# Performance work log

Measured on AMD Instinct MI355X. Metric: run time of the kernel, lower is better.

## Reference

```python
import jax, jax.numpy as jnp
import numpy as np
import math


def setup_inputs() -> dict:
    key = jax.random.key(0)
    k0, k1, k2, k3, k4 = jax.random.split(key, 5)
    in_f, out_f, nb = 512, 512, 8
    B, S = 4, 2048
    x = jax.random.normal(k0, (B, S, in_f), dtype=jnp.float32)
    # RBF params (frozen in original: basis_trainable=False)
    fan_in = in_f  # fan_in of rbf.weight.T which is (num_basis, in_features)
    bound = 1.0 / math.sqrt(fan_in)
    rbf_weight = jax.random.uniform(k1, (in_f, nb), dtype=jnp.float32,
                                    minval=-math.sqrt(3.0) * 0.33 / math.sqrt(fan_in),
                                    maxval=math.sqrt(3.0) * 0.33 / math.sqrt(fan_in))
    rbf_centers = jnp.tile(jnp.linspace(-bound, bound, nb, dtype=jnp.float32)[None, :], (in_f, 1))
    # KAN spline weight (in, nb, out); fan_in for init is in_f*nb
    fan2 = in_f * nb
    wb = math.sqrt(3.0) * 0.33 / math.sqrt(fan2)
    weight = jax.random.uniform(k2, (in_f, nb, out_f), dtype=jnp.float32, minval=-wb, maxval=wb)
    bias = jax.random.uniform(k3, (out_f,), dtype=jnp.float32,
                              minval=-1.0 / math.sqrt(fan2), maxval=1.0 / math.sqrt(fan2))
    scale_base = jax.random.uniform(k4, (in_f, out_f), dtype=jnp.float32, minval=-0.1, maxval=0.1)
    return {"x": x, "rbf_weight": rbf_weight, "rbf_centers": rbf_centers,
            "weight": weight, "bias": bias, "scale_base": scale_base}


def reference(x, rbf_weight, rbf_centers, weight, bias, scale_base):
    in_f = x.shape[-1]
    nb = rbf_weight.shape[1]
    beta = (nb / math.log2(nb)) ** 2  # get_rbf_width(2/nb, log2(nb))
    batch_shape = x.shape[:-1]
    xf = x.reshape(-1, in_f)  # (N, in)
    # RBF basis expansion: (N, in, nb)
    z = xf[:, :, None] * rbf_weight[None, :, :] - rbf_centers[None, :, :]
    phi = jnp.exp(-beta * (z * z))
    # spline contraction + base path, expressed as efficient contractions
    y = jnp.einsum('nib,ibo->no', phi, weight)
    y = y + bias + jnp.cos(xf) @ scale_base
    return y.reshape(*batch_shape, weight.shape[-1])
```

## Files before the change

kernel.cpp:

```cpp
#include <hip/hip_runtime.h>
#include <hip/hip_bf16.h>

typedef __attribute__((ext_vector_type(8))) short short8;
typedef __attribute__((ext_vector_type(4))) float f32x4;

#define IN_F 512
#define OUT_F 512
#define BM 64
#define BN 256
#define BK 64
#define PHI_STEPS 64
#define NSTEPS 72
#define NT 2
#define IMG_CHUNKS 2048
#define ACH 512
#define A_SH (BM * BK)
#define B_SH (BN * BK)
#define PART_ELEMS (8192 * OUT_F)
#define C2 (-10.2591705f)

__device__ __forceinline__ short f2bf(float f) {
  unsigned u = __builtin_bit_cast(unsigned, f);
  u += 0x7fffu + ((u >> 16) & 1u);
  return (short)(u >> 16);
}

__device__ __forceinline__ void glds16(const void* g, void* l) {
  __builtin_amdgcn_global_load_lds(
      (const __attribute__((address_space(1))) unsigned int*)g,
      (__attribute__((address_space(3))) unsigned int*)l, 16, 0, 0);
}

__device__ __forceinline__ float bsrc(const float* __restrict__ w,
                                      const float* __restrict__ sb,
                                      int k, int col) {
  return (k < IN_F * 8) ? w[(size_t)k * OUT_F + col]
                        : sb[(size_t)(k - IN_F * 8) * OUT_F + col];
}

__global__ void __launch_bounds__(256) prep_b(const float* __restrict__ w,
                                              const float* __restrict__ sb,
                                              short* __restrict__ img) {
  const int D = blockIdx.x * 256 + threadIdx.x;
  const int ci = D & (IMG_CHUNKS - 1);
  const int im = D >> 11;
  const int s = im % NSTEPS;
  const int nt = im / NSTEPS;
  const int n = ci >> 3, slot = ci & 7;
  const int oct = slot ^ (n & 7);
  const int col = nt * BN + n;
  short8 v;
#pragma unroll
  for (int j = 0; j < 8; ++j) v[j] = f2bf(bsrc(w, sb, s * 64 + oct * 8 + j, col));
  *(short8*)&img[(size_t)D * 8] = v;
}

__global__ void __launch_bounds__(256) prep_a(const float* __restrict__ x,
                                              const float* __restrict__ rw,
                                              const float* __restrict__ rc,
                                              short* __restrict__ aimg) {
  const int D = blockIdx.x * 256 + threadIdx.x;
  const int ci = D & (ACH - 1);
  const int rest = D >> 9;
  const int s = rest % NSTEPS;
  const int mb = rest / NSTEPS;
  const int m = ci >> 3, slot = ci & 7;
  const int oct = slot ^ (m & 7);
  const int row = mb * BM + m;
  short8 v;
  if (s < PHI_STEPS) {
    const int feat = s * 8 + oct;
    const float xv = x[(size_t)row * IN_F + feat];
    const float4 r0 = *(const float4*)(rw + feat * 8);
    const float4 r1 = *(const float4*)(rw + feat * 8 + 4);
    const float4 q0 = *(const float4*)(rc + feat * 8);
    const float4 q1 = *(const float4*)(rc + feat * 8 + 4);
    const float rwv[8] = {r0.x, r0.y, r0.z, r0.w, r1.x, r1.y, r1.z, r1.w};
    const float rcv[8] = {q0.x, q0.y, q0.z, q0.w, q1.x, q1.y, q1.z, q1.w};
#pragma unroll
    for (int j = 0; j < 8; ++j) {
      const float z = fmaf(xv, rwv[j], -rcv[j]);
      v[j] = f2bf(exp2f(C2 * z * z));
    }
  } else {
    const float* xp = x + (size_t)row * IN_F + (s - PHI_STEPS) * 64 + oct * 8;
    const float4 u0 = *(const float4*)xp, u1 = *(const float4*)(xp + 4);
    v[0] = f2bf(__cosf(u0.x)); v[1] = f2bf(__cosf(u0.y));
    v[2] = f2bf(__cosf(u0.z)); v[3] = f2bf(__cosf(u0.w));
    v[4] = f2bf(__cosf(u1.x)); v[5] = f2bf(__cosf(u1.y));
    v[6] = f2bf(__cosf(u1.z)); v[7] = f2bf(__cosf(u1.w));
  }
  *(short8*)&aimg[(size_t)D * 8] = v;
}

__global__ void __launch_bounds__(256) reduce_add(const float* __restrict__ part,
                                                  float* __restrict__ out) {
  const int n4 = PART_ELEMS / 4;
  const float4* p4 = (const float4*)part;
  float4* o4 = (float4*)out;
  for (int i = blockIdx.x * 256 + threadIdx.x; i < n4; i += gridDim.x * 256) {
    float4 a = o4[i];
    const float4 b = p4[i];
    a.x += b.x; a.y += b.y; a.z += b.z; a.w += b.w;
    o4[i] = a;
  }
}

template <int KS>
__global__ void __launch_bounds__(512, 4) kan_gemm(
    const short* __restrict__ aimg, const short* __restrict__ bimg,
    const float* __restrict__ bias, float* __restrict__ out,
    float* __restrict__ part) {
  constexpr int SPLC = NSTEPS / KS;
  __shared__ __align__(16) short A_lds[2][A_SH];
  __shared__ __align__(16) short B_lds[2][B_SH];

  const int t = threadIdx.x, lane = t & 63, wid = t >> 6;
  const int wm = wid >> 2, wn = wid & 3;
  const int l15 = lane & 15, kb = lane >> 4;
  const int mb = blockIdx.x, nt = blockIdx.y;
  const int ks = (KS > 1) ? blockIdx.z : 0;
  const int m0 = mb * BM, n0 = nt * BN, s0 = ks * SPLC;

  f32x4 acc[2][4];
#pragma unroll
  for (int i = 0; i < 2; ++i)
#pragma unroll
    for (int j = 0; j < 4; ++j) acc[i][j] = (f32x4){0.f, 0.f, 0.f, 0.f};

  const short* abase = aimg + (size_t)mb * NSTEPS * ACH * 8;
  const short* bbase = bimg + (size_t)nt * NSTEPS * IMG_CHUNKS * 8;

  auto stage = [&](int s, int buf) {
    const short* as = abase + ((size_t)s * ACH + wid * 64 + lane) * 8;
    glds16(as, &A_lds[buf][wid * 512]);
    const short* bs = bbase + ((size_t)s * IMG_CHUNKS + wid * 64 + lane) * 8;
#pragma unroll
    for (int c2 = 0; c2 < 4; ++c2)
      glds16(bs + (size_t)c2 * 512 * 8, &B_lds[buf][c2 * 4096 + wid * 512]);
  };

  auto mfma_step = [&](int buf) {
#pragma unroll
    for (int kk = 0; kk < 2; ++kk) {
      const int sk = kk * 4 + kb;
      short8 af[2], bf[4];
#pragma unroll
      for (int mi = 0; mi < 2; ++mi) {
        const int r = wm * 32 + mi * 16 + l15;
        af[mi] = *(const short8*)&A_lds[buf][r * BK + (sk ^ (r & 7)) * 8];
      }
#pragma unroll
      for (int ni = 0; ni < 4; ++ni) {
        const int n = wn * 64 + ni * 16 + l15;
        bf[ni] = *(const short8*)&B_lds[buf][n * BK + (sk ^ (n & 7)) * 8];
      }
#pragma unroll
      for (int mi = 0; mi < 2; ++mi)
#pragma unroll
        for (int ni = 0; ni < 4; ++ni)
          acc[mi][ni] = __builtin_amdgcn_mfma_f32_16x16x32_bf16(
              af[mi], bf[ni], acc[mi][ni], 0, 0, 0);
    }
  };

  stage(s0, 0);

  for (int si = 0; si < SPLC; ++si) {
    const int c = si & 1;
    if (si + 1 < SPLC) {
      stage(s0 + si + 1, c ^ 1);
      asm volatile("s_waitcnt vmcnt(5)" ::: "memory");
    } else {
      asm volatile("s_waitcnt vmcnt(0)" ::: "memory");
    }
    __builtin_amdgcn_s_barrier();
    mfma_step(c);
    __builtin_amdgcn_s_barrier();
  }

#pragma unroll
  for (int ni = 0; ni < 4; ++ni) {
    const int col = n0 + wn * 64 + ni * 16 + l15;
    const float bb = (KS == 1 || ks == 0) ? bias[col] : 0.f;
#pragma unroll
    for (int mi = 0; mi < 2; ++mi) {
      const int rb = m0 + wm * 32 + mi * 16 + kb * 4;
#pragma unroll
      for (int r4 = 0; r4 < 4; ++r4) {
        const size_t idx = (size_t)(rb + r4) * OUT_F + col;
        if (KS == 1 || ks == 0) out[idx] = acc[mi][ni][r4] + bb;
        else                    part[idx] = acc[mi][ni][r4];
      }
    }
  }
}

template <int KS, bool PREB>
__global__ void __launch_bounds__(256, 2) kan_fused(
    const float* __restrict__ x, const float* __restrict__ rw,
    const float* __restrict__ rc, const float* __restrict__ w,
    const float* __restrict__ bias, const float* __restrict__ sb,
    const short* __restrict__ bimg, float* __restrict__ out,
    float* __restrict__ part) {
  constexpr int SPLC = NSTEPS / KS;
  __shared__ __align__(16) short A_lds[2][A_SH];
  __shared__ __align__(16) short B_lds[2][B_SH];

  const int t = threadIdx.x, lane = t & 63, wid = t >> 6;
  const int l15 = lane & 15, kb = lane >> 4;
  const int m0 = blockIdx.x * BM;
  const int nt = blockIdx.y, n0 = nt * BN;
  const int ks = (KS > 1) ? blockIdx.z : 0;
  const int s0 = ks * SPLC;
  const int a_il = t & 7;
  const int a_m = t >> 3;

  f32x4 acc[4][4];
#pragma unroll
  for (int i = 0; i < 4; ++i)
#pragma unroll
    for (int j = 0; j < 4; ++j) acc[i][j] = (f32x4){0.f, 0.f, 0.f, 0.f};

  float xrA, xrB;
  float4 pr0, pr1, pc0, pc1;
  float4 cA0, cA1, cB0, cB1;

  auto loadNext = [&](int s1) {
    if (s1 < PHI_STEPS) {
      const int feat = s1 * 8 + a_il;
      xrA = x[(size_t)(m0 + a_m) * IN_F + feat];
      xrB = x[(size_t)(m0 + a_m + 32) * IN_F + feat];
      pr0 = *(const float4*)(rw + feat * 8);
      pr1 = *(const float4*)(rw + feat * 8 + 4);
      pc0 = *(const float4*)(rc + feat * 8);
      pc1 = *(const float4*)(rc + feat * 8 + 4);
    } else {
      const float* xpA = x + (size_t)(m0 + a_m) * IN_F + (s1 - PHI_STEPS) * 64 + a_il * 8;
      const float* xpB = xpA + (size_t)32 * IN_F;
      cA0 = *(const float4*)xpA; cA1 = *(const float4*)(xpA + 4);
      cB0 = *(const float4*)xpB; cB1 = *(const float4*)(xpB + 4);
    }
  };

  auto writeA = [&](int s1, short* __restrict__ Ad) {
    short8 avA, avB;
    if (s1 < PHI_STEPS) {
      const float rwv[8] = {pr0.x, pr0.y, pr0.z, pr0.w, pr1.x, pr1.y, pr1.z, pr1.w};
      const float rcv[8] = {pc0.x, pc0.y, pc0.z, pc0.w, pc1.x, pc1.y, pc1.z, pc1.w};
#pragma unroll
      for (int b = 0; b < 8; ++b) {
        const float zA = fmaf(xrA, rwv[b], -rcv[b]);
        const float zB = fmaf(xrB, rwv[b], -rcv[b]);
        avA[b] = f2bf(exp2f(C2 * zA * zA));
        avB[b] = f2bf(exp2f(C2 * zB * zB));
      }
    } else {
      avA[0] = f2bf(__cosf(cA0.x)); avA[1] = f2bf(__cosf(cA0.y));
      avA[2] = f2bf(__cosf(cA0.z)); avA[3] = f2bf(__cosf(cA0.w));
      avA[4] = f2bf(__cosf(cA1.x)); avA[5] = f2bf(__cosf(cA1.y));
      avA[6] = f2bf(__cosf(cA1.z)); avA[7] = f2bf(__cosf(cA1.w));
      avB[0] = f2bf(__cosf(cB0.x)); avB[1] = f2bf(__cosf(cB0.y));
      avB[2] = f2bf(__cosf(cB0.z)); avB[3] = f2bf(__cosf(cB0.w));
      avB[4] = f2bf(__cosf(cB1.x)); avB[5] = f2bf(__cosf(cB1.y));
      avB[6] = f2bf(__cosf(cB1.z)); avB[7] = f2bf(__cosf(cB1.w));
    }
    const int mA = a_m, mB = a_m + 32;
    *(short8*)&Ad[mA * BK + (a_il ^ (mA & 7)) * 8] = avA;
    *(short8*)&Ad[mB * BK + (a_il ^ (mB & 7)) * 8] = avB;
  };

  auto stageB = [&](int s, short* __restrict__ Bd) {
    if (PREB) {
      const short* src = bimg + ((size_t)(nt * NSTEPS + s) * IMG_CHUNKS + t) * 8;
#pragma unroll
      for (int c = 0; c < 8; ++c)
        glds16(src + (size_t)c * 256 * 8, Bd + c * 2048 + wid * 512);
    } else {
    }
  };

  auto mfma_half = [&](const short* __restrict__ Ab, const short* __restrict__ Bb,
                       int kk) {
    const int sk = kk * 4 + kb;
    short8 af[4], bf[4];
#pragma unroll
    for (int mi = 0; mi < 4; ++mi) {
      const int r = mi * 16 + l15;
      af[mi] = *(const short8*)&Ab[r * BK + (sk ^ (r & 7)) * 8];
    }
#pragma unroll
    for (int ni = 0; ni < 4; ++ni) {
      const int n = wid * 64 + ni * 16 + l15;
      bf[ni] = *(const short8*)&Bb[n * BK + (sk ^ (n & 7)) * 8];
    }
#pragma unroll
    for (int mi = 0; mi < 4; ++mi)
#pragma unroll
      for (int ni = 0; ni < 4; ++ni)
        acc[mi][ni] = __builtin_amdgcn_mfma_f32_16x16x32_bf16(
            af[mi], bf[ni], acc[mi][ni], 0, 0, 0);
  };

  stageB(s0, B_lds[0]);
  loadNext(s0);
  writeA(s0, A_lds[0]);
  __syncthreads();

  for (int si = 0; si < SPLC; ++si) {
    const int c = si & 1;
    const int s = s0 + si;
    if (si + 1 < SPLC) { stageB(s + 1, B_lds[c ^ 1]); loadNext(s + 1); }
    mfma_half(A_lds[c], B_lds[c], 0);
    if (si + 1 < SPLC) writeA(s + 1, A_lds[c ^ 1]);
    mfma_half(A_lds[c], B_lds[c], 1);
    __syncthreads();
  }

#pragma unroll
  for (int ni = 0; ni < 4; ++ni) {
    const int col = n0 + wid * 64 + ni * 16 + l15;
    const float bb = (KS == 1 || ks == 0) ? bias[col] : 0.f;
#pragma unroll
    for (int mi = 0; mi < 4; ++mi) {
      const int rb = m0 + mi * 16 + kb * 4;
#pragma unroll
      for (int r4 = 0; r4 < 4; ++r4) {
        const size_t idx = (size_t)(rb + r4) * OUT_F + col;
        if (KS == 1 || ks == 0) out[idx] = acc[mi][ni][r4] + bb;
        else                    part[idx] = acc[mi][ni][r4];
      }
    }
  }
}

extern "C" void kernel_launch(void* const* d_in, const int* in_sizes, int n_in,
                              void* d_out, int out_size, void* d_ws, size_t ws_size,
                              hipStream_t stream) {
  const float* x    = (const float*)d_in[0];
  const float* rw   = (const float*)d_in[1];
  const float* rc   = (const float*)d_in[2];
  const float* w    = (const float*)d_in[3];
  const float* bias = (const float*)d_in[4];
  const float* sb   = (const float*)d_in[5];
  float* out = (float*)d_out;

  const int nrows = in_sizes[0] / IN_F;
  const int mb = nrows / BM;

  const size_t bimg_bytes = (size_t)NT * NSTEPS * IMG_CHUNKS * 16;
  const size_t aimg_bytes = (size_t)mb * NSTEPS * ACH * 16;
  const size_t part_bytes = (size_t)PART_ELEMS * sizeof(float);

  const int bch = NT * NSTEPS * IMG_CHUNKS;
  const int ach_total = mb * NSTEPS * ACH;

  if (ws_size >= bimg_bytes + aimg_bytes + part_bytes) {
    short* bimg = (short*)d_ws;
    short* aimg = (short*)((char*)d_ws + bimg_bytes);
    float* part = (float*)((char*)d_ws + bimg_bytes + aimg_bytes);
    prep_b<<<bch / 256, 256, 0, stream>>>(w, sb, bimg);
    prep_a<<<ach_total / 256, 256, 0, stream>>>(x, rw, rc, aimg);
    kan_gemm<2><<<dim3(mb, NT, 2), 512, 0, stream>>>(aimg, bimg, bias, out, part);
    reduce_add<<<2048, 256, 0, stream>>>(part, out);
  } else if (ws_size >= bimg_bytes + aimg_bytes) {
    short* bimg = (short*)d_ws;
    short* aimg = (short*)((char*)d_ws + bimg_bytes);
    prep_b<<<bch / 256, 256, 0, stream>>>(w, sb, bimg);
    prep_a<<<ach_total / 256, 256, 0, stream>>>(x, rw, rc, aimg);
    kan_gemm<1><<<dim3(mb, NT, 1), 512, 0, stream>>>(aimg, bimg, bias, out, nullptr);
  } else if (ws_size >= bimg_bytes + part_bytes) {
    short* bimg = (short*)d_ws;
    float* part = (float*)((char*)d_ws + bimg_bytes);
    prep_b<<<bch / 256, 256, 0, stream>>>(w, sb, bimg);
    kan_fused<2, true><<<dim3(mb, NT, 2), 256, 0, stream>>>(x, rw, rc, w, bias, sb,
                                                            bimg, out, part);
    reduce_add<<<2048, 256, 0, stream>>>(part, out);
  } else {
    short* bimg = (short*)d_ws;
    prep_b<<<bch / 256, 256, 0, stream>>>(w, sb, bimg);
    kan_fused<1, true><<<dim3(mb, NT, 1), 256, 0, stream>>>(x, rw, rc, w, bias, sb,
                                                            bimg, out, nullptr);
  }
}
```

Baseline: 82.62 us.

## Retile precomputed-operand GEMM to 128x128 blocks with 4 waves

The main GEMM path changes from 64x256 tiles with 8 waves to 128x128 tiles with 4 waves. Each wave now computes a 64x64 sub-tile with 4x4 MFMA accumulators. The B image is re-laid out in 128-column panels and A is staged from two 64-row panels. The aim is to raise arithmetic intensity per LDS byte and balance A/B reuse, at the cost of more registers per thread and fewer blocks in the grid.

```diff
diff --git a/kernel.cpp b/kernel.cpp
--- a/kernel.cpp
+++ b/kernel.cpp
@@ -6,16 +6,15 @@
 
 #define IN_F 512
 #define OUT_F 512
-#define BM 64
-#define BN 256
 #define BK 64
 #define PHI_STEPS 64
 #define NSTEPS 72
-#define NT 2
-#define IMG_CHUNKS 2048
+#define PAN 64
 #define ACH 512
-#define A_SH (BM * BK)
-#define B_SH (BN * BK)
+#define BCH4 1024
+#define NT4 4
+#define BCH2 2048
+#define NT2 2
 #define PART_ELEMS (8192 * OUT_F)
 #define C2 (-10.2591705f)
 
@@ -38,17 +37,34 @@
                         : sb[(size_t)(k - IN_F * 8) * OUT_F + col];
 }
 
-__global__ void __launch_bounds__(256) prep_b(const float* __restrict__ w,
-                                              const float* __restrict__ sb,
-                                              short* __restrict__ img) {
+__global__ void __launch_bounds__(256) prep_b4(const float* __restrict__ w,
+                                               const float* __restrict__ sb,
+                                               short* __restrict__ img) {
   const int D = blockIdx.x * 256 + threadIdx.x;
-  const int ci = D & (IMG_CHUNKS - 1);
+  const int ci = D & (BCH4 - 1);
+  const int im = D >> 10;
+  const int s = im % NSTEPS;
+  const int nt = im / NSTEPS;
+  const int n = ci >> 3, slot = ci & 7;
+  const int oct = slot ^ (n & 7);
+  const int col = nt * 128 + n;
+  short8 v;
+#pragma unroll
+  for (int j = 0; j < 8; ++j) v[j] = f2bf(bsrc(w, sb, s * 64 + oct * 8 + j, col));
+  *(short8*)&img[(size_t)D * 8] = v;
+}
+
+__global__ void __launch_bounds__(256) prep_b2(const float* __restrict__ w,
+                                               const float* __restrict__ sb,
+                                               short* __restrict__ img) {
+  const int D = blockIdx.x * 256 + threadIdx.x;
+  const int ci = D & (BCH2 - 1);
   const int im = D >> 11;
   const int s = im % NSTEPS;
   const int nt = im / NSTEPS;
   const int n = ci >> 3, slot = ci & 7;
   const int oct = slot ^ (n & 7);
-  const int col = nt * BN + n;
+  const int col = nt * 256 + n;
   short8 v;
 #pragma unroll
   for (int j = 0; j < 8; ++j) v[j] = f2bf(bsrc(w, sb, s * 64 + oct * 8 + j, col));
@@ -63,10 +79,10 @@
   const int ci = D & (ACH - 1);
   const int rest = D >> 9;
   const int s = rest % NSTEPS;
-  const int mb = rest / NSTEPS;
+  const int pan = rest / NSTEPS;
   const int m = ci >> 3, slot = ci & 7;
   const int oct = slot ^ (m & 7);
-  const int row = mb * BM + m;
+  const int row = pan * PAN + m;
   short8 v;
   if (s < PHI_STEPS) {
     const int feat = s * 8 + oct;
@@ -107,47 +123,51 @@
 }
 
 template <int KS>
-__global__ void __launch_bounds__(512, 4) kan_gemm(
+__global__ void __launch_bounds__(256, 2) kan_gemm(
     const short* __restrict__ aimg, const short* __restrict__ bimg,
     const float* __restrict__ bias, float* __restrict__ out,
     float* __restrict__ part) {
   constexpr int SPLC = NSTEPS / KS;
-  __shared__ __align__(16) short A_lds[2][A_SH];
-  __shared__ __align__(16) short B_lds[2][B_SH];
+  __shared__ __align__(16) short A_lds[2][128 * BK];
+  __shared__ __align__(16) short B_lds[2][128 * BK];
 
   const int t = threadIdx.x, lane = t & 63, wid = t >> 6;
-  const int wm = wid >> 2, wn = wid & 3;
+  const int wm = wid >> 1, wn = wid & 1;
   const int l15 = lane & 15, kb = lane >> 4;
   const int mb = blockIdx.x, nt = blockIdx.y;
   const int ks = (KS > 1) ? blockIdx.z : 0;
-  const int m0 = mb * BM, n0 = nt * BN, s0 = ks * SPLC;
-
-  f32x4 acc[2][4];
-#pragma unroll
-  for (int i = 0; i < 2; ++i)
+  const int m0 = mb * 128, n0 = nt * 128, s0 = ks * SPLC;
+
+  f32x4 acc[4][4];
+#pragma unroll
+  for (int i = 0; i < 4; ++i)
 #pragma unroll
     for (int j = 0; j < 4; ++j) acc[i][j] = (f32x4){0.f, 0.f, 0.f, 0.f};
 
-  const short* abase = aimg + (size_t)mb * NSTEPS * ACH * 8;
-  const short* bbase = bimg + (size_t)nt * NSTEPS * IMG_CHUNKS * 8;
-
   auto stage = [&](int s, int buf) {
-    const short* as = abase + ((size_t)s * ACH + wid * 64 + lane) * 8;
-    glds16(as, &A_lds[buf][wid * 512]);
-    const short* bs = bbase + ((size_t)s * IMG_CHUNKS + wid * 64 + lane) * 8;
-#pragma unroll
-    for (int c2 = 0; c2 < 4; ++c2)
-      glds16(bs + (size_t)c2 * 512 * 8, &B_lds[buf][c2 * 4096 + wid * 512]);
+#pragma unroll
+    for (int c = 0; c < 4; ++c) {
+      const int p = c >> 1;
+      const short* src = aimg +
+          (((size_t)(2 * mb + p) * NSTEPS + s) * ACH + (c & 1) * 256 + wid * 64 + lane) * 8;
+      glds16(src, &A_lds[buf][c * 2048 + wid * 512]);
+    }
+#pragma unroll
+    for (int c = 0; c < 4; ++c) {
+      const short* src = bimg +
+          (((size_t)nt * NSTEPS + s) * BCH4 + c * 256 + wid * 64 + lane) * 8;
+      glds16(src, &B_lds[buf][c * 2048 + wid * 512]);
+    }
   };
 
   auto mfma_step = [&](int buf) {
 #pragma unroll
     for (int kk = 0; kk < 2; ++kk) {
       const int sk = kk * 4 + kb;
-      short8 af[2], bf[4];
-#pragma unroll
-      for (int mi = 0; mi < 2; ++mi) {
-        const int r = wm * 32 + mi * 16 + l15;
+      short8 af[4], bf[4];
+#pragma unroll
+      for (int mi = 0; mi < 4; ++mi) {
+        const int r = wm * 64 + mi * 16 + l15;
         af[mi] = *(const short8*)&A_lds[buf][r * BK + (sk ^ (r & 7)) * 8];
       }
 #pragma unroll
@@ -156,7 +176,7 @@
         bf[ni] = *(const short8*)&B_lds[buf][n * BK + (sk ^ (n & 7)) * 8];
       }
 #pragma unroll
-      for (int mi = 0; mi < 2; ++mi)
+      for (int mi = 0; mi < 4; ++mi)
 #pragma unroll
         for (int ni = 0; ni < 4; ++ni)
           acc[mi][ni] = __builtin_amdgcn_mfma_f32_16x16x32_bf16(
@@ -170,7 +190,7 @@
     const int c = si & 1;
     if (si + 1 < SPLC) {
       stage(s0 + si + 1, c ^ 1);
-      asm volatile("s_waitcnt vmcnt(5)" ::: "memory");
+      asm volatile("s_waitcnt vmcnt(8)" ::: "memory");
     } else {
       asm volatile("s_waitcnt vmcnt(0)" ::: "memory");
     }
@@ -184,8 +204,8 @@
     const int col = n0 + wn * 64 + ni * 16 + l15;
     const float bb = (KS == 1 || ks == 0) ? bias[col] : 0.f;
 #pragma unroll
-    for (int mi = 0; mi < 2; ++mi) {
-      const int rb = m0 + wm * 32 + mi * 16 + kb * 4;
+    for (int mi = 0; mi < 4; ++mi) {
+      const int rb = m0 + wm * 64 + mi * 16 + kb * 4;
 #pragma unroll
       for (int r4 = 0; r4 < 4; ++r4) {
         const size_t idx = (size_t)(rb + r4) * OUT_F + col;
@@ -196,25 +216,23 @@
   }
 }
 
-template <int KS, bool PREB>
+template <int KS>
 __global__ void __launch_bounds__(256, 2) kan_fused(
     const float* __restrict__ x, const float* __restrict__ rw,
-    const float* __restrict__ rc, const float* __restrict__ w,
-    const float* __restrict__ bias, const float* __restrict__ sb,
+    const float* __restrict__ rc, const float* __restrict__ bias,
     const short* __restrict__ bimg, float* __restrict__ out,
     float* __restrict__ part) {
   constexpr int SPLC = NSTEPS / KS;
-  __shared__ __align__(16) short A_lds[2][A_SH];
-  __shared__ __align__(16) short B_lds[2][B_SH];
+  __shared__ __align__(16) short A_lds[2][64 * BK];
+  __shared__ __align__(16) short B_lds[2][256 * BK];
 
   const int t = threadIdx.x, lane = t & 63, wid = t >> 6;
   const int l15 = lane & 15, kb = lane >> 4;
-  const int m0 = blockIdx.x * BM;
-  const int nt = blockIdx.y, n0 = nt * BN;
+  const int m0 = blockIdx.x * 64;
+  const int nt = blockIdx.y, n0 = nt * 256;
   const int ks = (KS > 1) ? blockIdx.z : 0;
   const int s0 = ks * SPLC;
-  const int a_il = t & 7;
-  const int a_m = t >> 3;
+  const int a_il = t & 7, a_m = t >> 3;
 
   f32x4 acc[4][4];
 #pragma unroll
@@ -223,8 +241,7 @@
     for (int j = 0; j < 4; ++j) acc[i][j] = (f32x4){0.f, 0.f, 0.f, 0.f};
 
   float xrA, xrB;
-  float4 pr0, pr1, pc0, pc1;
-  float4 cA0, cA1, cB0, cB1;
+  float4 pr0, pr1, pc0, pc1, cA0, cA1, cB0, cB1;
 
   auto loadNext = [&](int s1) {
     if (s1 < PHI_STEPS) {
@@ -271,13 +288,10 @@
   };
 
   auto stageB = [&](int s, short* __restrict__ Bd) {
-    if (PREB) {
-      const short* src = bimg + ((size_t)(nt * NSTEPS + s) * IMG_CHUNKS + t) * 8;
-#pragma unroll
-      for (int c = 0; c < 8; ++c)
-        glds16(src + (size_t)c * 256 * 8, Bd + c * 2048 + wid * 512);
-    } else {
-    }
+    const short* src = bimg + ((size_t)(nt * NSTEPS + s) * BCH2 + t) * 8;
+#pragma unroll
+    for (int c = 0; c < 8; ++c)
+      glds16(src + (size_t)c * 256 * 8, Bd + c * 2048 + wid * 512);
   };
 
   auto mfma_half = [&](const short* __restrict__ Ab, const short* __restrict__ Bb,
@@ -346,40 +360,38 @@
   float* out = (float*)d_out;
 
   const int nrows = in_sizes[0] / IN_F;
-  const int mb = nrows / BM;
-
-  const size_t bimg_bytes = (size_t)NT * NSTEPS * IMG_CHUNKS * 16;
-  const size_t aimg_bytes = (size_t)mb * NSTEPS * ACH * 16;
+  const int npan = nrows / PAN;
+
+  const size_t b4_bytes   = (size_t)NT4 * NSTEPS * BCH4 * 16;
+  const size_t b2_bytes   = (size_t)NT2 * NSTEPS * BCH2 * 16;
+  const size_t aimg_bytes = (size_t)npan * NSTEPS * ACH * 16;
   const size_t part_bytes = (size_t)PART_ELEMS * sizeof(float);
 
-  const int bch = NT * NSTEPS * IMG_CHUNKS;
-  const int ach_total = mb * NSTEPS * ACH;
-
-  if (ws_size >= bimg_bytes + aimg_bytes + part_bytes) {
+  if (ws_size >= b4_bytes + aimg_bytes + part_bytes) {
     short* bimg = (short*)d_ws;
-    short* aimg = (short*)((char*)d_ws + bimg_bytes);
-    float* part = (float*)((char*)d_ws + bimg_bytes + aimg_bytes);
-    prep_b<<<bch / 256, 256, 0, stream>>>(w, sb, bimg);
-    prep_a<<<ach_total / 256, 256, 0, stream>>>(x, rw, rc, aimg);
-    kan_gemm<2><<<dim3(mb, NT, 2), 512, 0, stream>>>(aimg, bimg, bias, out, part);
+    short* aimg = (short*)((char*)d_ws + b4_bytes);
+    float* part = (float*)((char*)d_ws + b4_bytes + aimg_bytes);
+    prep_b4<<<NT4 * NSTEPS * BCH4 / 256, 256, 0, stream>>>(w, sb, bimg);
+    prep_a<<<npan * NSTEPS * ACH / 256, 256, 0, stream>>>(x, rw, rc, aimg);
+    kan_gemm<2><<<dim3(nrows / 128, 4, 2), 256, 0, stream>>>(aimg, bimg, bias, out, part);
     reduce_add<<<2048, 256, 0, stream>>>(part, out);
-  } else if (ws_size >= bimg_bytes + aimg_bytes) {
+  } else if (ws_size >= b4_bytes + aimg_bytes) {
     short* bimg = (short*)d_ws;
-    short* aimg = (short*)((char*)d_ws + bimg_bytes);
-    prep_b<<<bch / 256, 256, 0, stream>>>(w, sb, bimg);
-    prep_a<<<ach_total / 256, 256, 0, stream>>>(x, rw, rc, aimg);
-    kan_gemm<1><<<dim3(mb, NT, 1), 512, 0, stream>>>(aimg, bimg, bias, out, nullptr);
-  } else if (ws_size >= bimg_bytes + part_bytes) {
+    short* aimg = (short*)((char*)d_ws + b4_bytes);
+    prep_b4<<<NT4 * NSTEPS * BCH4 / 256, 256, 0, stream>>>(w, sb, bimg);
+    prep_a<<<npan * NSTEPS * ACH / 256, 256, 0, stream>>>(x, rw, rc, aimg);
+    kan_gemm<1><<<dim3(nrows / 128, 4, 1), 256, 0, stream>>>(aimg, bimg, bias, out, nullptr);
+  } else if (ws_size >= b2_bytes + part_bytes) {
     short* bimg = (short*)d_ws;
-    float* part = (float*)((char*)d_ws + bimg_bytes);
-    prep_b<<<bch / 256, 256, 0, stream>>>(w, sb, bimg);
-    kan_fused<2, true><<<dim3(mb, NT, 2), 256, 0, stream>>>(x, rw, rc, w, bias, sb,
-                                                            bimg, out, part);
+    float* part = (float*)((char*)d_ws + b2_bytes);
+    prep_b2<<<NT2 * NSTEPS * BCH2 / 256, 256, 0, stream>>>(w, sb, bimg);
+    kan_fused<2><<<dim3(nrows / 64, NT2, 2), 256, 0, stream>>>(x, rw, rc, bias,
+                                                               bimg, out, part);
     reduce_add<<<2048, 256, 0, stream>>>(part, out);
   } else {
     short* bimg = (short*)d_ws;
-    prep_b<<<bch / 256, 256, 0, stream>>>(w, sb, bimg);
-    kan_fused<1, true><<<dim3(mb, NT, 1), 256, 0, stream>>>(x, rw, rc, w, bias, sb,
-                                                            bimg, out, nullptr);
-  }
-}
+    prep_b2<<<NT2 * NSTEPS * BCH2 / 256, 256, 0, stream>>>(w, sb, bimg);
+    kan_fused<1><<<dim3(nrows / 64, NT2, 1), 256, 0, stream>>>(x, rw, rc, bias,
+                                                               bimg, out, nullptr);
+  }
+}
```

Result: no change. 83.28 us (+0.8%).
